# Optimization experiments

Hardware: AMD Instinct MI355X
Metric: run time of the kernel (lower is better)

Reference implementation:

```python
import jax, jax.numpy as jnp
import numpy as np

DEPTH = 5  # init kwarg


def setup_inputs() -> dict:
    key = jax.random.key(0)
    ks = jax.random.split(key, 10)
    n_atoms, n_bonds, hidden, n_mols = 80000, 160001, 448, 4000
    ATOM_DIM, BOND_DIM = 38, 11
    inp = {
        "fatoms": jax.random.normal(ks[0], (n_atoms, ATOM_DIM), jnp.float32),
        "fbonds": jax.random.normal(ks[1], (n_bonds, ATOM_DIM + BOND_DIM), jnp.float32),
        "W_i": jax.random.normal(ks[2], (ATOM_DIM + BOND_DIM, hidden), jnp.float32) * 0.1,
        "W_h": jax.random.normal(ks[3], (hidden, hidden), jnp.float32) * 0.05,
        "W_o": jax.random.normal(ks[4], (ATOM_DIM + hidden, hidden), jnp.float32) * 0.05,
        "b_o": jax.random.normal(ks[5], (hidden,), jnp.float32),
        "agraph": jax.random.randint(ks[6], (n_atoms, 6), 0, n_bonds, jnp.int64),
        "bgraph": jax.random.randint(ks[7], (n_bonds, 6), 0, n_bonds, jnp.int64),
        "mol_idx": jnp.sort(jax.random.randint(ks[8], (n_atoms,), 0, n_mols, jnp.int64)),
        "n_mols": n_mols,
    }
    return inp


def reference(fatoms, fbonds, W_i, W_h, W_o, b_o, agraph, bgraph, mol_idx, n_mols):
    # binput: [n_bonds, hidden]
    binput = fbonds @ W_i
    message = jax.nn.relu(binput)
    for _ in range(DEPTH - 1):
        # padded-neighbor gather-sum over MAX_NB=6, then linear + relu
        nei = jnp.take(message, bgraph, axis=0).sum(axis=1)  # [n_bonds, hidden]
        message = jax.nn.relu(binput + nei @ W_h)
    # atom readout
    nei = jnp.take(message, agraph, axis=0).sum(axis=1)  # [n_atoms, hidden]
    ainput = jnp.concatenate([fatoms, nei], axis=1)
    atom_hiddens = jax.nn.relu(ainput @ W_o + b_o)
    # per-molecule mean pooling (scope -> segment ids)
    sums = jax.ops.segment_sum(atom_hiddens, mol_idx, num_segments=n_mols)
    counts = jax.ops.segment_sum(jnp.ones((atom_hiddens.shape[0],), atom_hiddens.dtype), mol_idx, num_segments=n_mols)
    return sums / jnp.maximum(counts, 1.0)[:, None]
```

## Files before the change

### kernel.cpp

```cpp
#include <hip/hip_runtime.h>

#define HIDDEN 448

typedef __attribute__((ext_vector_type(8))) short short8;
typedef __attribute__((ext_vector_type(4))) float f32x4;

__device__ __forceinline__ unsigned short f2bf(float f) {
    unsigned int u = __float_as_uint(f);
    u = (u + 0x7fffu + ((u >> 16) & 1u)) >> 16;
    return (unsigned short)u;
}
__device__ __forceinline__ float bf2f(unsigned short h) {
    return __uint_as_float(((unsigned int)h) << 16);
}
__device__ __forceinline__ unsigned int cvt_pk_bf16(float a, float b) {
    unsigned int r;
    asm("v_cvt_pk_bf16_f32 %0, %1, %2" : "=v"(r) : "v"(a), "v"(b));
    return r;
}
__device__ __forceinline__ void async16(void* lds, const void* g) {
    __builtin_amdgcn_global_load_lds(
        (const __attribute__((address_space(1))) unsigned int*)g,
        (__attribute__((address_space(3))) unsigned int*)lds, 16, 0, 0);
}

__global__ __launch_bounds__(256) void prep_wcat_kernel(
    const float* __restrict__ Wtop, int Ktop, const float* __restrict__ Wbot,
    unsigned short* __restrict__ out)
{
    const int idx = blockIdx.x * 256 + threadIdx.x;
    if (idx >= 448 * 512) return;
    const int n = idx >> 9, k = idx & 511;
    float v = 0.0f;
    if (k < Ktop) v = Wtop[k * HIDDEN + n];
    else if (k >= 64) v = Wbot[(k - 64) * HIDDEN + n];
    out[(size_t)n * 512 + (k ^ (((n >> 1) & 3) << 3))] = f2bf(v);
}

__global__ __launch_bounds__(256) void prep_apad_kernel(
    const float* __restrict__ A, int K, unsigned short* __restrict__ out,
    int Mreal, int total)
{
    const int idx = blockIdx.x * 256 + threadIdx.x;
    if (idx >= total) return;
    const int row = idx >> 6, k = idx & 63;
    const float v = (row < Mreal && k < K) ? A[(size_t)row * K + k] : 0.0f;
    out[(size_t)row * 64 + (k ^ (((row >> 1) & 3) << 3))] = f2bf(v);
}

template<int GRAPH, int OUTQ>
__global__ __launch_bounds__(512, 4) void gemm_mfma_kernel(
    const unsigned short* __restrict__ Apad,
    const unsigned char* __restrict__ Xq,
    const float* __restrict__ Xs,
    const int* __restrict__ graph,
    const unsigned short* __restrict__ BT,
    const float* __restrict__ bias,
    unsigned short* outh,
    unsigned char* __restrict__ outq,
    float* __restrict__ outs,
    int M, int nsteps)
{
    __shared__ __align__(16) unsigned char smem[33792];
    unsigned short* As = (unsigned short*)smem;
    unsigned short* Bs = (unsigned short*)(smem + 4096);
    float* rmaxbuf = (float*)(smem + 32768);

    const int tid = threadIdx.x, lane = tid & 63, wv = tid >> 6;
    const int row0 = blockIdx.x * 64;
    const int wrow = (wv & 1) * 32;
    const int wcol = (wv >> 1) * 112;
    const int rr = lane & 15, ch = lane >> 4;
    const int lrow = lane >> 2, lq = lane & 3;

    const int arow = tid >> 3, asub = tid & 7;
    int goff[6]; float gscl[6];
    if (GRAPH) {
        const int grow = row0 + arow;
        const bool ok = grow < M;
        #pragma unroll
        for (int j = 0; j < 6; ++j) {
            const int gj = ok ? graph[(size_t)grow * 6 + j] : 0;
            goff[j] = gj * 448;
            gscl[j] = ok ? Xs[gj] : 0.0f;
        }
    }
    const int awaddr = arow * 32 + (((asub >> 1) ^ ((arow >> 1) & 3)) << 3)
                     + (asub & 1) * 4;

    f32x4 acc[2][7] = {};

    for (int s = 0; s < nsteps; ++s) {
        #pragma unroll
        for (int i = 0; i < 4; ++i) {
            const int t = wv + 8 * i;
            if (t < 28)
                async16(Bs + t * 512 + lane * 8,
                        BT + (size_t)(t * 16 + lrow) * 512 + s * 32 + lq * 8);
        }
        if (s < 2) {
            if (wv >= 4) {
                const int a = wv - 4;
                const int grow = row0 + a * 16 + lrow;
                async16(As + a * 512 + lane * 8,
                        Apad + (size_t)grow * 64 + s * 32 + lq * 8);
            }
        } else if (GRAPH) {
            const int colb = (s - 2) * 32 + asub * 4;
            float a0 = 0, a1 = 0, a2 = 0, a3 = 0;
            #pragma unroll
            for (int j = 0; j < 6; ++j) {
                const unsigned int b = *(const unsigned int*)(Xq + goff[j] + colb);
                const float sc = gscl[j];
                a0 += (float)(b & 255u) * sc;
                a1 += (float)((b >> 8) & 255u) * sc;
                a2 += (float)((b >> 16) & 255u) * sc;
                a3 += (float)(b >> 24) * sc;
            }
            *(uint2*)&As[awaddr] = make_uint2(cvt_pk_bf16(a0, a1),
                                              cvt_pk_bf16(a2, a3));
        }
        __syncthreads();

        short8 av[2];
        #pragma unroll
        for (int m = 0; m < 2; ++m) {
            const int r = wrow + m * 16 + rr;
            av[m] = *(const short8*)&As[r * 32 + ((ch ^ ((r >> 1) & 3)) << 3)];
        }
        #pragma unroll
        for (int n = 0; n < 7; ++n) {
            const int cl = wcol + n * 16 + rr;
            const short8 bv = *(const short8*)&Bs[cl * 32 + ((ch ^ ((cl >> 1) & 3)) << 3)];
            #pragma unroll
            for (int m = 0; m < 2; ++m)
                acc[m][n] = __builtin_amdgcn_mfma_f32_16x16x32_bf16(
                    av[m], bv, acc[m][n], 0, 0, 0);
        }
        __syncthreads();
    }

    const int r4 = ch << 2;

    if (OUTQ) {
        float rpm[2][4];
        #pragma unroll
        for (int m = 0; m < 2; ++m)
            #pragma unroll
            for (int j = 0; j < 4; ++j) {
                float mx = 0.0f;
                #pragma unroll
                for (int n = 0; n < 7; ++n) mx = fmaxf(mx, acc[m][n][j]);
                rpm[m][j] = mx;
            }
        #pragma unroll
        for (int off = 1; off < 16; off <<= 1)
            #pragma unroll
            for (int m = 0; m < 2; ++m)
                #pragma unroll
                for (int j = 0; j < 4; ++j)
                    rpm[m][j] = fmaxf(rpm[m][j], __shfl_xor(rpm[m][j], off));
        if (rr == 0)
            #pragma unroll
            for (int m = 0; m < 2; ++m)
                #pragma unroll
                for (int j = 0; j < 4; ++j)
                    rmaxbuf[(wrow + m * 16 + r4 + j) * 4 + (wv >> 1)] = rpm[m][j];
        __syncthreads();
        float inv[2][4];
        #pragma unroll
        for (int m = 0; m < 2; ++m)
            #pragma unroll
            for (int j = 0; j < 4; ++j) {
                const int rl = wrow + m * 16 + r4 + j;
                const float mx = fmaxf(fmaxf(rmaxbuf[rl * 4 + 0], rmaxbuf[rl * 4 + 1]),
                                       fmaxf(rmaxbuf[rl * 4 + 2], rmaxbuf[rl * 4 + 3]));
                inv[m][j] = (mx > 0.0f) ? (255.0f / mx) : 0.0f;
                if (wv < 2 && rr == 0 && row0 + rl < M)
                    outs[row0 + rl] = mx * (1.0f / 255.0f);
            }
        unsigned char* q8 = smem;
        #pragma unroll
        for (int m = 0; m < 2; ++m)
            #pragma unroll
            for (int j = 0; j < 4; ++j) {
                const int rl = wrow + m * 16 + r4 + j;
                #pragma unroll
                for (int n = 0; n < 7; ++n) {
                    const float v = fmaxf(acc[m][n][j], 0.0f);
                    q8[rl * 448 + wcol + n * 16 + rr] =
                        (unsigned char)__float2uint_rn(fminf(v * inv[m][j], 255.0f));
                }
            }
        __syncthreads();
        #pragma unroll
        for (int i = 0; i < 4; ++i) {
            const int u = tid + 512 * i;
            if (u < 1792 && row0 + u / 28 < M)
                ((uint4*)(outq + (size_t)row0 * 448))[u] = ((const uint4*)q8)[u];
        }
    } else {
        #pragma unroll
        for (int n = 0; n < 7; ++n) {
            const int col = wcol + n * 16 + rr;
            const float bsv = bias ? bias[col] : 0.0f;
            #pragma unroll
            for (int m = 0; m < 2; ++m)
                #pragma unroll
                for (int j = 0; j < 4; ++j) {
                    const int row = row0 + wrow + m * 16 + r4 + j;
                    if (row < M)
                        outh[(size_t)row * HIDDEN + col] =
                            f2bf(fmaxf(acc[m][n][j] + bsv, 0.0f));
                }
        }
    }
}

__global__ void segmean_kernel(
    const unsigned short* __restrict__ ah, const int* __restrict__ mol_idx,
    float* __restrict__ out, int n_atoms)
{
    const int m = blockIdx.x;
    const int c = threadIdx.x;
    int l = 0, r = n_atoms;
    while (l < r) { const int mid = (l + r) >> 1; if (mol_idx[mid] < m) l = mid + 1; else r = mid; }
    const int start = l;
    r = n_atoms;
    while (l < r) { const int mid = (l + r) >> 1; if (mol_idx[mid] < m + 1) l = mid + 1; else r = mid; }
    const int end = l;
    float acc = 0.0f;
    for (int a = start; a < end; ++a) acc += bf2f(ah[(size_t)a * HIDDEN + c]);
    out[(size_t)m * HIDDEN + c] = acc / fmaxf((float)(end - start), 1.0f);
}

__global__ __launch_bounds__(256) void fill_kernel(float* __restrict__ out, int n, float val)
{
    const int i = blockIdx.x * 256 + threadIdx.x;
    if (i < n) out[i] = val;
}

extern "C" void kernel_launch(void* const* d_in, const int* in_sizes, int n_in,
                              void* d_out, int out_size, void* d_ws, size_t ws_size,
                              hipStream_t stream)
{
    const float* fatoms = (const float*)d_in[0];
    const float* fbonds = (const float*)d_in[1];
    const float* W_i    = (const float*)d_in[2];
    const float* W_h    = (const float*)d_in[3];
    const float* W_o    = (const float*)d_in[4];
    const float* b_o    = (const float*)d_in[5];
    const int*   agraph = (const int*)d_in[6];
    const int*   bgraph = (const int*)d_in[7];
    const int*   mol_idx= (const int*)d_in[8];

    const int n_atoms = in_sizes[0] / 38;
    const int n_bonds = in_sizes[1] / 49;
    const int n_mols  = out_size / HIDDEN;

    const int Mb_b = (n_bonds + 63) & ~63;
    const int Mb_a = (n_atoms + 63) & ~63;

    const size_t eW  = (size_t)448 * 512;
    const size_t eFb = (size_t)Mb_b * 64;
    const size_t eFa = (size_t)Mb_a * 64;
    const size_t eX  = (size_t)Mb_b * 448;

    const size_t need = 2 * eW * 2 + eFb * 2 + eFa * 2 +
                        2 * eX + 2 * (size_t)Mb_b * 4;

    const dim3 blk(256);

    if (ws_size >= need) {
        unsigned short* WhcatT  = (unsigned short*)d_ws;
        unsigned short* WocatT  = WhcatT + eW;
        unsigned short* fbondsP = WocatT + eW;
        unsigned short* fatomsP = fbondsP + eFb;
        unsigned char*  Xq0     = (unsigned char*)(fatomsP + eFa);
        unsigned char*  Xq1     = Xq0 + eX;
        float*          Xs0     = (float*)(Xq1 + eX);
        float*          Xs1     = Xs0 + Mb_b;

        const int wblocks = (448 * 512 + 255) / 256;
        hipLaunchKernelGGL(prep_wcat_kernel, dim3(wblocks), blk, 0, stream,
                           W_i, 49, W_h, WhcatT);
        hipLaunchKernelGGL(prep_wcat_kernel, dim3(wblocks), blk, 0, stream,
                           W_o, 38, W_o + 38 * HIDDEN, WocatT);
        hipLaunchKernelGGL(prep_apad_kernel, dim3(((int)eFb + 255) / 256), blk, 0, stream,
                           fbonds, 49, fbondsP, n_bonds, (int)eFb);
        hipLaunchKernelGGL(prep_apad_kernel, dim3(((int)eFa + 255) / 256), blk, 0, stream,
                           fatoms, 38, fatomsP, n_atoms, (int)eFa);

        const dim3 gB(Mb_b / 64), gA(Mb_a / 64), tpb(512);

        unsigned char* Xq[2] = {Xq0, Xq1};
        float*         Xs[2] = {Xs0, Xs1};

        hipLaunchKernelGGL((gemm_mfma_kernel<0, 1>), gB, tpb, 0, stream,
                           fbondsP, (const unsigned char*)nullptr, (const float*)nullptr,
                           (const int*)nullptr, WhcatT, (const float*)nullptr,
                           (unsigned short*)nullptr, Xq[0], Xs[0], n_bonds, 2);
        int p = 0;
        for (int it = 0; it < 4; ++it) {
            hipLaunchKernelGGL((gemm_mfma_kernel<1, 1>), gB, tpb, 0, stream,
                               fbondsP, Xq[p], Xs[p], bgraph, WhcatT,
                               (const float*)nullptr, (unsigned short*)nullptr,
                               Xq[p ^ 1], Xs[p ^ 1], n_bonds, 16);
            p ^= 1;
        }
        unsigned short* ah = (unsigned short*)Xq[p ^ 1];
        hipLaunchKernelGGL((gemm_mfma_kernel<1, 0>), gA, tpb, 0, stream,
                           fatomsP, Xq[p], Xs[p], agraph, WocatT, b_o,
                           ah, (unsigned char*)nullptr, (float*)nullptr, n_atoms, 16);
        hipLaunchKernelGGL(segmean_kernel, dim3(n_mols), dim3(HIDDEN), 0, stream,
                           ah, mol_idx, (float*)d_out, n_atoms);
    } else {
        const float val = -(float)((double)ws_size / (1024.0 * 1024.0));
        hipLaunchKernelGGL(fill_kernel, dim3((out_size + 255) / 256), blk, 0, stream,
                           (float*)d_out, out_size, val);
    }
}
```

Baseline: 968.0 us.

## Prefetch gathered int8 neighbor rows and build 64-wide A tiles every other step

The graph-gather path now loads 8 bytes per neighbor into registers one stage ahead (software prefetch) and builds a 64-column A tile in LDS every two k-steps instead of 32 columns each step. The dense A input is loaded once at step 0 for both halves. This aims to hide gather latency behind the MFMA loop and cut per-step gather overhead. In exchange it doubles A LDS usage, adds 12 registers for prefetch, and adds a barrier before reusing smem for quantized output.

```diff
diff --git a/kernel.cpp b/kernel.cpp
--- a/kernel.cpp
+++ b/kernel.cpp
@@ -61,10 +61,10 @@
     float* __restrict__ outs,
     int M, int nsteps)
 {
-    __shared__ __align__(16) unsigned char smem[33792];
+    __shared__ __align__(16) unsigned char smem[37888];
     unsigned short* As = (unsigned short*)smem;
-    unsigned short* Bs = (unsigned short*)(smem + 4096);
-    float* rmaxbuf = (float*)(smem + 32768);
+    unsigned short* Bs = (unsigned short*)(smem + 8192);
+    float* rmaxbuf = (float*)(smem + 36864);
 
     const int tid = threadIdx.x, lane = tid & 63, wv = tid >> 6;
     const int row0 = blockIdx.x * 64;
@@ -74,7 +74,11 @@
     const int lrow = lane >> 2, lq = lane & 3;
 
     const int arow = tid >> 3, asub = tid & 7;
+    const int ah = asub >> 2, ac = asub & 3;
+    const int awaddr = arow * 64 + ah * 32 + ((ac ^ ((arow >> 1) & 3)) << 3);
+
     int goff[6]; float gscl[6];
+    uint2 pf[6];
     if (GRAPH) {
         const int grow = row0 + arow;
         const bool ok = grow < M;
@@ -84,9 +88,10 @@
             goff[j] = gj * 448;
             gscl[j] = ok ? Xs[gj] : 0.0f;
         }
+        #pragma unroll
+        for (int j = 0; j < 6; ++j)
+            pf[j] = *(const uint2*)(Xq + goff[j] + asub * 8);
     }
-    const int awaddr = arow * 32 + (((asub >> 1) ^ ((arow >> 1) & 3)) << 3)
-                     + (asub & 1) * 4;
 
     f32x4 acc[2][7] = {};
 
@@ -98,35 +103,48 @@
                 async16(Bs + t * 512 + lane * 8,
                         BT + (size_t)(t * 16 + lrow) * 512 + s * 32 + lq * 8);
         }
-        if (s < 2) {
-            if (wv >= 4) {
-                const int a = wv - 4;
-                const int grow = row0 + a * 16 + lrow;
-                async16(As + a * 512 + lane * 8,
-                        Apad + (size_t)grow * 64 + s * 32 + lq * 8);
-            }
-        } else if (GRAPH) {
-            const int colb = (s - 2) * 32 + asub * 4;
-            float a0 = 0, a1 = 0, a2 = 0, a3 = 0;
+        if (s == 0) {
+            async16(As + wv * 512 + lane * 8,
+                    Apad + (size_t)(row0 + wv * 8) * 64 + lane * 8);
+        } else if (GRAPH && s >= 2 && !((s - 2) & 1)) {
+            const uint2 b0 = pf[0], b1 = pf[1], b2 = pf[2],
+                        b3 = pf[3], b4 = pf[4], b5 = pf[5];
+            float a0 = 0, a1 = 0, a2 = 0, a3 = 0, a4 = 0, a5 = 0, a6 = 0, a7 = 0;
             #pragma unroll
             for (int j = 0; j < 6; ++j) {
-                const unsigned int b = *(const unsigned int*)(Xq + goff[j] + colb);
+                const uint2 b = (j == 0) ? b0 : (j == 1) ? b1 : (j == 2) ? b2
+                              : (j == 3) ? b3 : (j == 4) ? b4 : b5;
                 const float sc = gscl[j];
-                a0 += (float)(b & 255u) * sc;
-                a1 += (float)((b >> 8) & 255u) * sc;
-                a2 += (float)((b >> 16) & 255u) * sc;
-                a3 += (float)(b >> 24) * sc;
-            }
-            *(uint2*)&As[awaddr] = make_uint2(cvt_pk_bf16(a0, a1),
-                                              cvt_pk_bf16(a2, a3));
-        }
-        __syncthreads();
-
+                a0 += (float)(b.x & 255u) * sc;
+                a1 += (float)((b.x >> 8) & 255u) * sc;
+                a2 += (float)((b.x >> 16) & 255u) * sc;
+                a3 += (float)(b.x >> 24) * sc;
+                a4 += (float)(b.y & 255u) * sc;
+                a5 += (float)((b.y >> 8) & 255u) * sc;
+                a6 += (float)((b.y >> 16) & 255u) * sc;
+                a7 += (float)(b.y >> 24) * sc;
+            }
+            uint4 w;
+            w.x = cvt_pk_bf16(a0, a1);
+            w.y = cvt_pk_bf16(a2, a3);
+            w.z = cvt_pk_bf16(a4, a5);
+            w.w = cvt_pk_bf16(a6, a7);
+            *(uint4*)&As[awaddr] = w;
+            const int nxt = ((s - 2) >> 1) + 1;
+            if (nxt < 7) {
+                #pragma unroll
+                for (int j = 0; j < 6; ++j)
+                    pf[j] = *(const uint2*)(Xq + goff[j] + nxt * 64 + asub * 8);
+            }
+        }
+        __syncthreads();
+
+        const int hoff = (s & 1) * 32;
         short8 av[2];
         #pragma unroll
         for (int m = 0; m < 2; ++m) {
             const int r = wrow + m * 16 + rr;
-            av[m] = *(const short8*)&As[r * 32 + ((ch ^ ((r >> 1) & 3)) << 3)];
+            av[m] = *(const short8*)&As[r * 64 + hoff + ((ch ^ ((r >> 1) & 3)) << 3)];
         }
         #pragma unroll
         for (int n = 0; n < 7; ++n) {
@@ -179,6 +197,7 @@
                 if (wv < 2 && rr == 0 && row0 + rl < M)
                     outs[row0 + rl] = mx * (1.0f / 255.0f);
             }
+        __syncthreads();
         unsigned char* q8 = smem;
         #pragma unroll
         for (int m = 0; m < 2; ++m)
```

Result: faster. 928.3 us (-4.1%).
